# Performance work log

Hardware: AMD Instinct MI355X
Metric: run time of the kernel (lower is better)

The kernel has to match this reference:

```python
import jax, jax.numpy as jnp
import numpy as np

N = 50000; E = 200000; H = 128; L = 3; T = 2; FOUT = 64
G = 1000; NP = 3; ATOM_V = 64; BOND_V = 8
EPS = 1e-5
_DEG_HIST = np.array([0., 50000., 75000., 50000., 25000.])
# PyG PNAConv: avg_deg['log'] = sum(hist[d] * log(d+1)) / num_nodes
AVG_DEG_LOG = float((np.log(np.arange(5) + 1.0) * _DEG_HIST).sum() / _DEG_HIST.sum())


def _bn(v, g, b):
    # training-mode BatchNorm1d (biased variance), eps=1e-5
    mu = v.mean(0)
    var = ((v - mu) ** 2).mean(0)
    return (v - mu) * jax.lax.rsqrt(var + EPS) * g + b


def setup_inputs() -> dict:
    key = jax.random.key(0)
    ks = jax.random.split(key, 16)
    def nrm(k, shape, fan):
        return (jax.random.normal(k, shape, dtype=jnp.float32) / np.sqrt(fan)).astype(jnp.float32)
    return {
        'x': jax.random.randint(ks[0], (N, 9), 0, ATOM_V),
        'edge_index': jax.random.randint(ks[1], (2, E), 0, N),
        'batch': jnp.sort(jax.random.randint(ks[2], (N,), 0, G)),
        'edge_attr_idx': jax.random.randint(ks[3], (E, 3), 0, BOND_V),
        'atom_emb': nrm(ks[4], (9, ATOM_V, H), H),
        'bond_emb': nrm(ks[5], (3, BOND_V, H), H),
        'edge_W': nrm(ks[6], (L, H, H), H), 'edge_b': jnp.zeros((L, H), jnp.float32),
        'pre_W': nrm(ks[7], (L, T, 3 * H, H), 3 * H), 'pre_b': jnp.zeros((L, T, H), jnp.float32),
        'post_W': nrm(ks[8], (L, T, 13 * H, FOUT), 13 * H), 'post_b': jnp.zeros((L, T, FOUT), jnp.float32),
        'lin_W': nrm(ks[9], (L, H, H), H), 'lin_b': jnp.zeros((L, H), jnp.float32),
        'bn_g': jnp.ones((L, H), jnp.float32), 'bn_b': jnp.zeros((L, H), jnp.float32),
        'mlp_W': nrm(ks[10], (2, H, H), H), 'mlp_b': jnp.zeros((2, H), jnp.float32),
        'mlp_g': jnp.ones((2, H), jnp.float32), 'mlp_be': jnp.zeros((2, H), jnp.float32),
        'hW1': nrm(ks[11], (H, H // 2), H), 'hb1': jnp.zeros((H // 2,), jnp.float32),
        'hg1': jnp.ones((H // 2,), jnp.float32), 'hbe1': jnp.zeros((H // 2,), jnp.float32),
        'hW2': nrm(ks[12], (H // 2, H // 4), H // 2), 'hb2': jnp.zeros((H // 4,), jnp.float32),
        'hg2': jnp.ones((H // 4,), jnp.float32), 'hbe2': jnp.zeros((H // 4,), jnp.float32),
        'hW3': nrm(ks[13], (H // 4, NP), H // 4), 'hb3': jnp.zeros((NP,), jnp.float32),
    }


def reference(x, edge_index, batch, edge_attr_idx, atom_emb, bond_emb,
              edge_W, edge_b, pre_W, pre_b, post_W, post_b, lin_W, lin_b,
              bn_g, bn_b, mlp_W, mlp_b, mlp_g, mlp_be,
              hW1, hb1, hg1, hbe1, hW2, hb2, hg2, hbe2, hW3, hb3):
    # encoders: sum of per-feature embeddings (OGB Atom/Bond encoder)
    h = atom_emb[jnp.arange(9), x].sum(1)               # [N,H]
    e = bond_emb[jnp.arange(3), edge_attr_idx].sum(1)   # [E,H]
    src, dst = edge_index[0], edge_index[1]
    cnt = jax.ops.segment_sum(jnp.ones((E,), jnp.float32), dst, N)
    deg = jnp.maximum(cnt, 1.0)[:, None, None]          # clamp(1), as in PyG scalers
    amp = jnp.log(deg + 1.0) / AVG_DEG_LOG
    att = AVG_DEG_LOG / jnp.log(deg + 1.0)
    has = (cnt > 0)[:, None, None]
    for l in range(L):
        ea = e @ edge_W[l] + edge_b[l]                                  # [E,H]
        msg_in = jnp.concatenate([h[dst], h[src], ea], -1)              # [E,3H]
        m = jnp.einsum('ef,tfh->eth', msg_in, pre_W[l]) + pre_b[l]      # [E,T,H]
        s1 = jax.ops.segment_sum(m, dst, N)
        s2 = jax.ops.segment_sum(m * m, dst, N)
        mean = s1 / deg
        std = jnp.sqrt(jax.nn.relu(s2 / deg - mean * mean) + EPS)
        mn = jnp.where(has, jax.ops.segment_min(m, dst, N), 0.0)
        mx = jnp.where(has, jax.ops.segment_max(m, dst, N), 0.0)
        agg = jnp.concatenate([mean, mn, mx, std], -1)                  # [N,T,4H]
        scaled = jnp.concatenate([agg, agg * amp, agg * att], -1)       # [N,T,12H]
        upd = jnp.concatenate(
            [jnp.broadcast_to(h[:, None, :], (N, T, H)), scaled], -1)   # [N,T,13H]
        o = jnp.einsum('ntf,tfo->nto', upd, post_W[l]) + post_b[l]      # [N,T,FOUT]
        o = o.reshape(N, T * FOUT) @ lin_W[l] + lin_b[l]                # [N,H]
        h = jax.nn.relu(_bn(o, bn_g[l], bn_b[l]))
    g = jax.ops.segment_sum(h, batch, G)                                # [G,H]
    for i in range(2):
        g = jax.nn.relu(_bn(g @ mlp_W[i] + mlp_b[i], mlp_g[i], mlp_be[i]))
    g = jax.nn.relu(_bn(g @ hW1 + hb1, hg1, hbe1))
    g = jax.nn.relu(_bn(g @ hW2 + hb2, hg2, hbe2))
    return g @ hW3 + hb3                                                # [G,NP]
```

## Files before the change

### kernel.cpp

```cpp
#include <hip/hip_runtime.h>
#include <math.h>


#define NN 50000
#define NE 200000
#define HD 128
#define NG 1000
#define EPSV 1e-5f
#define ALOGC 1.1330197327247628f

#define AP 1288
#define OP 136
#define ECAP 512
#define SCB 49

typedef __bf16 bf16x8 __attribute__((ext_vector_type(8)));
typedef float f32x4 __attribute__((ext_vector_type(4)));

__device__ __forceinline__ unsigned short f2bf(float f) {
    unsigned int u = __float_as_uint(f);
    unsigned int r = (u + 0x7FFFu + ((u >> 16) & 1u)) >> 16;
    return (unsigned short)r;
}
__device__ __forceinline__ float bf2f(unsigned short h) {
    return __uint_as_float((unsigned int)h << 16);
}

__global__ void k_fill(float* __restrict__ o, float v, int n) {
    int i = blockIdx.x * 256 + threadIdx.x;
    if (i < n) o[i] = v;
}

__global__ void k_zero(float* __restrict__ z, int n) {
    int i = blockIdx.x * 256 + threadIdx.x;
    if (i < n) z[i] = 0.f;
}

__global__ void k_encode_nodes(const int* __restrict__ x, const float* __restrict__ aemb,
                               float* __restrict__ h) {
    int n = blockIdx.x, c = threadIdx.x;
    __shared__ int xi[9];
    if (c < 9) xi[c] = x[n * 9 + c];
    __syncthreads();
    float acc = 0.f;
#pragma unroll
    for (int f = 0; f < 9; ++f) acc += aemb[(f * 64 + xi[f]) * HD + c];
    h[(size_t)n * HD + c] = acc;
}

__global__ void k_count(const int* __restrict__ dst, int* __restrict__ cnt) {
    int e = blockIdx.x * 256 + threadIdx.x;
    if (e < NE) atomicAdd(&cnt[dst[e]], 1);
}

__global__ __launch_bounds__(1024) void k_scanA(const int* __restrict__ cnt,
                                                int* __restrict__ sc, int* __restrict__ tot) {
    __shared__ int buf[1024];
    int tid = threadIdx.x;
    int i = blockIdx.x * 1024 + tid;
    int v = (i < NN) ? cnt[i] : 0;
    buf[tid] = v;
    __syncthreads();
    for (int s = 1; s < 1024; s <<= 1) {
        int t = (tid >= s) ? buf[tid - s] : 0;
        __syncthreads();
        buf[tid] += t;
        __syncthreads();
    }
    if (i < NN) sc[i] = buf[tid];
    if (tid == 1023) tot[blockIdx.x] = buf[1023];
}

__global__ void k_scanB(const int* __restrict__ tot, int* __restrict__ offb) {
    if (threadIdx.x == 0) {
        int run = 0;
        for (int b = 0; b < SCB; ++b) { offb[b] = run; run += tot[b]; }
    }
}

__global__ __launch_bounds__(1024) void k_scanC(
    const int* __restrict__ cnt, const int* __restrict__ sc, const int* __restrict__ offb,
    int* __restrict__ rowptr, float* __restrict__ ampv, float* __restrict__ attv) {
    int i = blockIdx.x * 1024 + threadIdx.x;
    if (i == 0) rowptr[0] = 0;
    if (i < NN) {
        rowptr[i + 1] = offb[blockIdx.x] + sc[i];
        int v = cnt[i];
        float dg = (float)(v > 0 ? v : 1);
        float lg = logf(dg + 1.0f);
        ampv[i] = lg / ALOGC;
        attv[i] = ALOGC / lg;
    }
}

__global__ void k_scatter(const int* __restrict__ dst, const int* __restrict__ rowptr,
                          int* __restrict__ fill, int* __restrict__ eperm) {
    int e = blockIdx.x * 256 + threadIdx.x;
    if (e < NE) {
        int d = dst[e];
        int pos = rowptr[d] + atomicAdd(&fill[d], 1);
        eperm[pos] = e;
    }
}

__global__ void k_eprep(const int* __restrict__ ei, const int* __restrict__ eai,
                        const int* __restrict__ eperm, int* __restrict__ precs) {
    int p = blockIdx.x * 256 + threadIdx.x;
    if (p < NE) {
        int e = eperm[p];
        int cidx = eai[e * 3] | (eai[e * 3 + 1] << 3) | (eai[e * 3 + 2] << 6);
        precs[p] = ei[e] | (cidx << 17);
    }
}

__global__ void k_fold(const float* __restrict__ edge_W, const float* __restrict__ edge_b,
                       const float* __restrict__ pre_W, const float* __restrict__ pre_b,
                       float* __restrict__ cW, float* __restrict__ tb) {
    int l = blockIdx.y;
    int k = blockIdx.x;
    int tj = threadIdx.x;
    int t = tj >> 7, j = tj & 127;
    const float* pw = pre_W + ((size_t)(l * 2 + t) * 384 + 256) * 128 + j;
    if (k < 128) {
        const float* ew = edge_W + ((size_t)l * 128 + k) * 128;
        float acc = 0.f;
        for (int i = 0; i < 128; ++i) acc += ew[i] * pw[i * 128];
        cW[((size_t)l * 128 + k) * 256 + tj] = acc;
    } else {
        const float* eb = edge_b + l * 128;
        float acc = pre_b[(l * 2 + t) * 128 + j];
        for (int i = 0; i < 128; ++i) acc += eb[i] * pw[i * 128];
        tb[l * 256 + tj] = acc;
    }
}

__global__ void k_bond(const float* __restrict__ bemb, const float* __restrict__ cW,
                       float* __restrict__ bondc) {
    int v = blockIdx.x, f = blockIdx.y, l = blockIdx.z;
    int tj = threadIdx.x;
    const float* src = bemb + (size_t)(f * 8 + v) * 128;
    const float* w = cW + (size_t)l * 128 * 256;
    float acc = 0.f;
    for (int i = 0; i < 128; ++i) acc += src[i] * w[i * 256 + tj];
    bondc[(((size_t)l * 3 + f) * 8 + v) * 256 + tj] = acc;
}

__global__ void k_bcomb(const float* __restrict__ bondc, float* __restrict__ bcomb) {
    int ci = blockIdx.x, l = blockIdx.y, tj = threadIdx.x;
    const float* base = bondc + (size_t)l * 3 * 8 * 256;
    float v = base[((0 * 8) + (ci & 7)) * 256 + tj]
            + base[((1 * 8) + ((ci >> 3) & 7)) * 256 + tj]
            + base[((2 * 8) + (ci >> 6)) * 256 + tj];
    bcomb[((size_t)l * 512 + ci) * 256 + tj] = v;
}

__global__ void k_pack(const float* __restrict__ W, int N, int NT,
                       unsigned short* __restrict__ pk) {
    int blk = blockIdx.x;
    int kstep = blk / NT, nt = blk - kstep * NT;
    int lane = threadIdx.x;
    int kb = kstep * 32 + (lane >> 4) * 8;
    int col = nt * 16 + (lane & 15);
    unsigned short tmp[8];
#pragma unroll
    for (int i = 0; i < 8; ++i) tmp[i] = f2bf(W[(size_t)(kb + i) * N + col]);
    *(uint4*)(pk + ((size_t)blk * 64 + lane) * 8) = *(uint4*)tmp;
}

__global__ void k_pack_pre(const float* __restrict__ preW,
                           unsigned short* __restrict__ phi,
                           unsigned short* __restrict__ plo) {
    int b = blockIdx.x;
    int kstep = b >> 5, nt = b & 31;
    int lane = threadIdx.x;
    int q = lane >> 4, nc = lane & 15;
    int col = nt * 16 + nc;
    int t = (col >> 7) & 1;
    int jcol = col & 127;
    int fbase = (col < 256) ? 0 : 128;
    unsigned short hi[8], lo[8];
#pragma unroll
    for (int i = 0; i < 8; ++i) {
        int k = kstep * 32 + q * 8 + i;
        float w = preW[((size_t)t * 384 + fbase + k) * 128 + jcol];
        unsigned short h16 = f2bf(w);
        hi[i] = h16;
        lo[i] = f2bf(w - bf2f(h16));
    }
    size_t base = ((size_t)b * 64 + lane) * 8;
    *(uint4*)(phi + base) = *(uint4*)hi;
    *(uint4*)(plo + base) = *(uint4*)lo;
}

__device__ __forceinline__ void pre_mfma_body(
    const unsigned short* __restrict__ ah, const unsigned short* __restrict__ al,
    const unsigned short* __restrict__ phi, const unsigned short* __restrict__ plo,
    const float* __restrict__ tb, int n0, int tid,
    float* __restrict__ hzd, float* __restrict__ hzs) {
    int lane = tid & 63, w = tid >> 6;
    int q = lane >> 4, nc = lane & 15;
    f32x4 acc[8];
#pragma unroll
    for (int j = 0; j < 8; ++j) acc[j] = (f32x4){0.f, 0.f, 0.f, 0.f};
#pragma unroll
    for (int kk = 0; kk < 4; ++kk) {
        bf16x8 Ahi = *(const bf16x8*)(ah + nc * 136 + kk * 32 + q * 8);
        bf16x8 Alo = *(const bf16x8*)(al + nc * 136 + kk * 32 + q * 8);
#pragma unroll
        for (int j = 0; j < 8; ++j) {
            int nt = w * 8 + j;
            size_t base = ((size_t)(kk * 32 + nt) * 64 + lane) * 8;
            bf16x8 Bhi = *(const bf16x8*)(phi + base);
            bf16x8 Blo = *(const bf16x8*)(plo + base);
            acc[j] = __builtin_amdgcn_mfma_f32_16x16x32_bf16(Ahi, Bhi, acc[j], 0, 0, 0);
            acc[j] = __builtin_amdgcn_mfma_f32_16x16x32_bf16(Ahi, Blo, acc[j], 0, 0, 0);
            acc[j] = __builtin_amdgcn_mfma_f32_16x16x32_bf16(Alo, Bhi, acc[j], 0, 0, 0);
        }
    }
#pragma unroll
    for (int j = 0; j < 8; ++j) {
        int col = (w * 8 + j) * 16 + nc;
#pragma unroll
        for (int reg = 0; reg < 4; ++reg) {
            int row = n0 + q * 4 + reg;
            if (col < 256) hzd[(size_t)row * 256 + col] = acc[j][reg] + tb[col];
            else           hzs[(size_t)row * 256 + (col - 256)] = acc[j][reg];
        }
    }
}

__global__ __launch_bounds__(256) void k_pre_m(
    const float* __restrict__ h,
    const unsigned short* __restrict__ phi, const unsigned short* __restrict__ plo,
    const float* __restrict__ tb,
    float* __restrict__ hzd, float* __restrict__ hzs) {
    __shared__ __align__(16) unsigned short ah[16 * 136];
    __shared__ __align__(16) unsigned short al[16 * 136];
    int n0 = blockIdx.x * 16;
    int tid = threadIdx.x;
    {
        int node = tid >> 4, cg = (tid & 15) * 8;
        const float* hs = h + (size_t)(n0 + node) * HD + cg;
        float4 v0 = *(const float4*)(hs);
        float4 v1 = *(const float4*)(hs + 4);
        float vv[8] = {v0.x, v0.y, v0.z, v0.w, v1.x, v1.y, v1.z, v1.w};
        unsigned short hh[8], ll[8];
#pragma unroll
        for (int i = 0; i < 8; ++i) {
            hh[i] = f2bf(vv[i]);
            ll[i] = f2bf(vv[i] - bf2f(hh[i]));
        }
        *(uint4*)(ah + node * 136 + cg) = *(uint4*)hh;
        *(uint4*)(al + node * 136 + cg) = *(uint4*)ll;
    }
    __syncthreads();
    pre_mfma_body(ah, al, phi, plo, tb, n0, tid, hzd, hzs);
}

__global__ __launch_bounds__(256) void k_bnpre(
    const float* __restrict__ o2, const float* __restrict__ stats,
    const float* __restrict__ g, const float* __restrict__ b,
    const unsigned short* __restrict__ phi, const unsigned short* __restrict__ plo,
    const float* __restrict__ tb,
    float* __restrict__ h, float* __restrict__ hzd, float* __restrict__ hzs) {
    __shared__ __align__(16) unsigned short ah[16 * 136];
    __shared__ __align__(16) unsigned short al[16 * 136];
    int n0 = blockIdx.x * 16;
    int tid = threadIdx.x;
    {
        int node = tid >> 4, cg = (tid & 15) * 8;
        int n = n0 + node;
        const float* os = o2 + (size_t)n * HD + cg;
        float4 v0 = *(const float4*)(os);
        float4 v1 = *(const float4*)(os + 4);
        float vv[8] = {v0.x, v0.y, v0.z, v0.w, v1.x, v1.y, v1.z, v1.w};
        unsigned short hh[8], ll[8];
        float ou[8];
#pragma unroll
        for (int i = 0; i < 8; ++i) {
            int c = cg + i;
            float mu = stats[c] * (1.f / NN);
            float var = stats[128 + c] * (1.f / NN) - mu * mu;
            float val = (vv[i] - mu) * rsqrtf(var + EPSV) * g[c] + b[c];
            val = fmaxf(val, 0.f);
            ou[i] = val;
            hh[i] = f2bf(val);
            ll[i] = f2bf(val - bf2f(hh[i]));
        }
        float* hd = h + (size_t)n * HD + cg;
        *(float4*)(hd) = make_float4(ou[0], ou[1], ou[2], ou[3]);
        *(float4*)(hd + 4) = make_float4(ou[4], ou[5], ou[6], ou[7]);
        *(uint4*)(ah + node * 136 + cg) = *(uint4*)hh;
        *(uint4*)(al + node * 136 + cg) = *(uint4*)ll;
    }
    __syncthreads();
    pre_mfma_body(ah, al, phi, plo, tb, n0, tid, hzd, hzs);
}

__global__ __launch_bounds__(256) void k_post(
    const float* __restrict__ h,
    const float* __restrict__ hzd, const float* __restrict__ hzs,
    const int* __restrict__ rowptr, const int* __restrict__ precs,
    const float* __restrict__ bcomb,
    const float* __restrict__ ampv, const float* __restrict__ attv,
    const unsigned short* __restrict__ pkPost,
    const float* __restrict__ postb,
    const unsigned short* __restrict__ pkLin,
    const float* __restrict__ linb,
    float* __restrict__ o2, float* __restrict__ stats) {
    __shared__ __align__(16) unsigned short a_lds[16 * AP];
    __shared__ __align__(16) unsigned short o_lds[16 * OP];
    __shared__ int es[ECAP];
    __shared__ float s_amp[16], s_att[16];
    int n0 = blockIdx.x * 16;
    int tid = threadIdx.x;

    int pbase = rowptr[n0];
    int ecount = rowptr[n0 + 16] - pbase;
    for (int i = tid; i < ecount && i < ECAP; i += 256) es[i] = precs[pbase + i];
    {
        int node = tid >> 4, cg = (tid & 15) * 8;
        const float* hs = h + (size_t)(n0 + node) * HD + cg;
        float4 v0 = *(const float4*)(hs);
        float4 v1 = *(const float4*)(hs + 4);
        unsigned short* d0 = a_lds + node * AP + cg;
        unsigned short* d1 = d0 + 640;
        unsigned short bb[8];
        bb[0] = f2bf(v0.x); bb[1] = f2bf(v0.y); bb[2] = f2bf(v0.z); bb[3] = f2bf(v0.w);
        bb[4] = f2bf(v1.x); bb[5] = f2bf(v1.y); bb[6] = f2bf(v1.z); bb[7] = f2bf(v1.w);
#pragma unroll
        for (int i = 0; i < 8; ++i) { d0[i] = bb[i]; d1[i] = bb[i]; }
    }
    if (tid < 16) { s_amp[tid] = ampv[n0 + tid]; s_att[tid] = attv[n0 + tid]; }
    __syncthreads();

    {
        int wv = tid >> 6, lane = tid & 63;
        int cc = lane * 4;
        int tt = cc >> 7, jj = cc & 127;
        bool incap = (ecount <= ECAP);
        const float4 Z4 = make_float4(0.f, 0.f, 0.f, 0.f);
        for (int i = 0; i < 4; ++i) {
            int r = wv * 4 + i;
            int n = n0 + r;
            int p0 = rowptr[n], p1 = rowptr[n + 1];
            float4 hd = *(const float4*)(hzd + (size_t)n * 256 + cc);
            float4 s1 = Z4, s2 = Z4;
            float4 mn = make_float4(3.4e38f, 3.4e38f, 3.4e38f, 3.4e38f);
            float4 mx = make_float4(-3.4e38f, -3.4e38f, -3.4e38f, -3.4e38f);
            for (int p = p0; p < p1; ++p) {
                int rec = incap ? es[p - pbase] : precs[p];
                int sp = rec & 131071;
                int ci = rec >> 17;
                float4 vs = *(const float4*)(hzs + (size_t)sp * 256 + cc);
                float4 bc = *(const float4*)(bcomb + (size_t)ci * 256 + cc);
                float wx = vs.x + bc.x, wy = vs.y + bc.y, wz = vs.z + bc.z, ww = vs.w + bc.w;
                s1.x += wx; s1.y += wy; s1.z += wz; s1.w += ww;
                s2.x += wx * wx; s2.y += wy * wy; s2.z += wz * wz; s2.w += ww * ww;
                mn.x = fminf(mn.x, wx); mn.y = fminf(mn.y, wy);
                mn.z = fminf(mn.z, wz); mn.w = fminf(mn.w, ww);
                mx.x = fmaxf(mx.x, wx); mx.y = fmaxf(mx.y, wy);
                mx.z = fmaxf(mx.z, wz); mx.w = fmaxf(mx.w, ww);
            }
            int cnt = p1 - p0;
            float inv = 1.f / (float)(cnt > 0 ? cnt : 1);
            float4 mw, stdv, mean;
            mw.x = s1.x * inv; mw.y = s1.y * inv; mw.z = s1.z * inv; mw.w = s1.w * inv;
            stdv.x = sqrtf(fmaxf(s2.x * inv - mw.x * mw.x, 0.f) + EPSV);
            stdv.y = sqrtf(fmaxf(s2.y * inv - mw.y * mw.y, 0.f) + EPSV);
            stdv.z = sqrtf(fmaxf(s2.z * inv - mw.z * mw.z, 0.f) + EPSV);
            stdv.w = sqrtf(fmaxf(s2.w * inv - mw.w * mw.w, 0.f) + EPSV);
            if (cnt > 0) {
                mean.x = hd.x + mw.x; mean.y = hd.y + mw.y;
                mean.z = hd.z + mw.z; mean.w = hd.w + mw.w;
                mn.x += hd.x; mn.y += hd.y; mn.z += hd.z; mn.w += hd.w;
                mx.x += hd.x; mx.y += hd.y; mx.z += hd.z; mx.w += hd.w;
            } else {
                mean = Z4; mn = Z4; mx = Z4;
            }
            unsigned short* d = a_lds + r * AP + tt * 640 + 128 + jj;
            d[0] = f2bf(mean.x); d[1] = f2bf(mean.y); d[2] = f2bf(mean.z); d[3] = f2bf(mean.w);
            d += 128; d[0] = f2bf(mn.x); d[1] = f2bf(mn.y); d[2] = f2bf(mn.z); d[3] = f2bf(mn.w);
            d += 128; d[0] = f2bf(mx.x); d[1] = f2bf(mx.y); d[2] = f2bf(mx.z); d[3] = f2bf(mx.w);
            d += 128; d[0] = f2bf(stdv.x); d[1] = f2bf(stdv.y); d[2] = f2bf(stdv.z); d[3] = f2bf(stdv.w);
        }
    }
    __syncthreads();

    {
        int lane = tid & 63;
        int w = tid >> 6;
        int t = w >> 1;
        int ntb = (w & 1) * 2;
        int q = lane >> 4, nc = lane & 15;
        const unsigned short* arow = a_lds + (size_t)nc * AP + t * 640 + q * 8;
        const unsigned short* pkt = pkPost + (size_t)t * 106496;
        f32x4 aP0 = {0.f, 0.f, 0.f, 0.f}, aP1 = {0.f, 0.f, 0.f, 0.f};
        f32x4 aA0 = {0.f, 0.f, 0.f, 0.f}, aA1 = {0.f, 0.f, 0.f, 0.f};
        f32x4 aT0 = {0.f, 0.f, 0.f, 0.f}, aT1 = {0.f, 0.f, 0.f, 0.f};
        for (int kk = 0; kk < 20; ++kk) {
            bf16x8 af = *(const bf16x8*)(arow + kk * 32);
            const unsigned short* pb = pkt + ((size_t)(kk * 4 + ntb) * 64 + lane) * 8;
            aP0 = __builtin_amdgcn_mfma_f32_16x16x32_bf16(af, *(const bf16x8*)(pb), aP0, 0, 0, 0);
            aP1 = __builtin_amdgcn_mfma_f32_16x16x32_bf16(af, *(const bf16x8*)(pb + 512), aP1, 0, 0, 0);
            if (kk >= 4) {
                const unsigned short* pa = pkt + ((size_t)((kk + 16) * 4 + ntb) * 64 + lane) * 8;
                aA0 = __builtin_amdgcn_mfma_f32_16x16x32_bf16(af, *(const bf16x8*)(pa), aA0, 0, 0, 0);
                aA1 = __builtin_amdgcn_mfma_f32_16x16x32_bf16(af, *(const bf16x8*)(pa + 512), aA1, 0, 0, 0);
                const unsigned short* pt = pkt + ((size_t)((kk + 32) * 4 + ntb) * 64 + lane) * 8;
                aT0 = __builtin_amdgcn_mfma_f32_16x16x32_bf16(af, *(const bf16x8*)(pt), aT0, 0, 0, 0);
                aT1 = __builtin_amdgcn_mfma_f32_16x16x32_bf16(af, *(const bf16x8*)(pt + 512), aT1, 0, 0, 0);
            }
        }
#pragma unroll
        for (int u = 0; u < 2; ++u) {
            int nt = ntb + u;
            int col = t * 64 + nt * 16 + nc;
            float pbia = postb[t * 64 + nt * 16 + nc];
            f32x4 P = u ? aP1 : aP0;
            f32x4 A = u ? aA1 : aA0;
            f32x4 T = u ? aT1 : aT0;
#pragma unroll
            for (int reg = 0; reg < 4; ++reg) {
                int mrow = q * 4 + reg;
                float val = P[reg] + s_amp[mrow] * A[reg] + s_att[mrow] * T[reg] + pbia;
                o_lds[mrow * OP + col] = f2bf(val);
            }
        }
    }
    __syncthreads();

    {
        int lane = tid & 63;
        int w = tid >> 6;
        int ntb = w * 2;
        int q = lane >> 4, nc = lane & 15;
        const unsigned short* arow = o_lds + (size_t)nc * OP + q * 8;
        f32x4 L0 = {0.f, 0.f, 0.f, 0.f}, L1 = {0.f, 0.f, 0.f, 0.f};
#pragma unroll
        for (int kk = 0; kk < 4; ++kk) {
            bf16x8 af = *(const bf16x8*)(arow + kk * 32);
            const unsigned short* pb = pkLin + ((size_t)(kk * 8 + ntb) * 64 + lane) * 8;
            L0 = __builtin_amdgcn_mfma_f32_16x16x32_bf16(af, *(const bf16x8*)(pb), L0, 0, 0, 0);
            L1 = __builtin_amdgcn_mfma_f32_16x16x32_bf16(af, *(const bf16x8*)(pb + 512), L1, 0, 0, 0);
        }
#pragma unroll
        for (int u = 0; u < 2; ++u) {
            int col = (ntb + u) * 16 + nc;
            float lb = linb[col];
            f32x4 L = u ? L1 : L0;
            float ps = 0.f, pss = 0.f;
#pragma unroll
            for (int reg = 0; reg < 4; ++reg) {
                int mrow = q * 4 + reg;
                float v = L[reg] + lb;
                o2[(size_t)(n0 + mrow) * HD + col] = v;
                ps += v; pss += v * v;
            }
            ps += __shfl_down(ps, 16); ps += __shfl_down(ps, 32);
            pss += __shfl_down(pss, 16); pss += __shfl_down(pss, 32);
            if (q == 0) {
                atomicAdd(&stats[col], ps);
                atomicAdd(&stats[128 + col], pss);
            }
        }
    }
}

__global__ void k_bn_relu(const float* __restrict__ o2, const float* __restrict__ stats,
                          const float* __restrict__ g, const float* __restrict__ b,
                          float* __restrict__ h) {
    int idx = blockIdx.x * 256 + threadIdx.x;
    int c = idx & 127;
    float mu = stats[c] * (1.f / NN);
    float var = stats[128 + c] * (1.f / NN) - mu * mu;
    float v = (o2[idx] - mu) * rsqrtf(var + EPSV) * g[c] + b[c];
    h[idx] = fmaxf(v, 0.f);
}

__global__ void k_pool(const float* __restrict__ h, const int* __restrict__ batch,
                       float* __restrict__ g0) {
    int c = threadIdx.x;
    int nbase = blockIdx.x * 64;
    float run = 0.f; int cur = -1;
    for (int i = 0; i < 64; ++i) {
        int n = nbase + i;
        if (n >= NN) break;
        int bb = batch[n];
        if (bb != cur) {
            if (cur >= 0) atomicAdd(&g0[(size_t)cur * HD + c], run);
            cur = bb; run = 0.f;
        }
        run += h[(size_t)n * HD + c];
    }
    if (cur >= 0) atomicAdd(&g0[(size_t)cur * HD + c], run);
}

__global__ void k_head_gemm(const float* __restrict__ x, const float* __restrict__ W,
                            const float* __restrict__ b, float* __restrict__ y,
                            float* __restrict__ stats, int K, int Kout) {
    int row = blockIdx.x;
    int col = threadIdx.x;
    if (col >= Kout) return;
    float acc = b[col];
    for (int k = 0; k < K; k += 4) {
        float4 xv = *(const float4*)(x + (size_t)row * K + k);
        acc += xv.x * W[(k + 0) * Kout + col] + xv.y * W[(k + 1) * Kout + col]
             + xv.z * W[(k + 2) * Kout + col] + xv.w * W[(k + 3) * Kout + col];
    }
    y[(size_t)row * Kout + col] = acc;
    if (stats) {
        atomicAdd(&stats[col], acc);
        atomicAdd(&stats[Kout + col], acc * acc);
    }
}

__global__ __launch_bounds__(128) void k_head_fused(
    const float* __restrict__ y_in, const float* __restrict__ stats_in,
    const float* __restrict__ g, const float* __restrict__ b,
    const float* __restrict__ W, const float* __restrict__ bias,
    float* __restrict__ y_out, float* __restrict__ stats_out, int Kin, int Kout) {
    __shared__ float row[128];
    int r = blockIdx.x, tid = threadIdx.x;
    if (tid < Kin) {
        float mu = stats_in[tid] * (1.f / NG);
        float var = stats_in[Kin + tid] * (1.f / NG) - mu * mu;
        float v = (y_in[(size_t)r * Kin + tid] - mu) * rsqrtf(var + EPSV) * g[tid] + b[tid];
        row[tid] = fmaxf(v, 0.f);
    }
    __syncthreads();
    if (tid < Kout) {
        float acc = bias[tid];
        for (int k = 0; k < Kin; ++k) acc += row[k] * W[(size_t)k * Kout + tid];
        y_out[(size_t)r * Kout + tid] = acc;
        if (stats_out) {
            atomicAdd(&stats_out[tid], acc);
            atomicAdd(&stats_out[Kout + tid], acc * acc);
        }
    }
}

extern "C" void kernel_launch(void* const* d_in, const int* in_sizes, int n_in,
                              void* d_out, int out_size, void* d_ws, size_t ws_size,
                              hipStream_t stream) {
    const int*   x        = (const int*)  d_in[0];
    const int*   ei       = (const int*)  d_in[1];
    const int*   batch    = (const int*)  d_in[2];
    const int*   eai      = (const int*)  d_in[3];
    const float* atom_emb = (const float*)d_in[4];
    const float* bond_emb = (const float*)d_in[5];
    const float* edge_W   = (const float*)d_in[6];
    const float* edge_b   = (const float*)d_in[7];
    const float* pre_W    = (const float*)d_in[8];
    const float* pre_b    = (const float*)d_in[9];
    const float* post_W   = (const float*)d_in[10];
    const float* post_b   = (const float*)d_in[11];
    const float* lin_W    = (const float*)d_in[12];
    const float* lin_b    = (const float*)d_in[13];
    const float* bn_g     = (const float*)d_in[14];
    const float* bn_b     = (const float*)d_in[15];
    const float* mlp_W    = (const float*)d_in[16];
    const float* mlp_b    = (const float*)d_in[17];
    const float* mlp_g    = (const float*)d_in[18];
    const float* mlp_be   = (const float*)d_in[19];
    const float* hW1 = (const float*)d_in[20]; const float* hb1  = (const float*)d_in[21];
    const float* hg1 = (const float*)d_in[22]; const float* hbe1 = (const float*)d_in[23];
    const float* hW2 = (const float*)d_in[24]; const float* hb2  = (const float*)d_in[25];
    const float* hg2 = (const float*)d_in[26]; const float* hbe2 = (const float*)d_in[27];
    const float* hW3 = (const float*)d_in[28]; const float* hb3  = (const float*)d_in[29];
    float* out = (float*)d_out;
    (void)n_in; (void)in_sizes;

    char* p = (char*)d_ws;
    size_t off = 0;
    auto alloc = [&](size_t bytes) -> char* {
        char* r = p + off;
        off += (bytes + 255) & ~(size_t)255;
        return r;
    };
    float* h     = (float*)alloc((size_t)NN * HD * 4);
    float* o2    = (float*)alloc((size_t)NN * HD * 4);
    float* hzd   = (float*)alloc((size_t)NN * 256 * 4);
    float* hzs   = (float*)alloc((size_t)NN * 256 * 4);
    float* ampv  = (float*)alloc((size_t)NN * 4);
    float* attv  = (float*)alloc((size_t)NN * 4);
    int*   rowptr= (int*)  alloc((size_t)(NN + 1) * 4);
    int*   eperm = (int*)  alloc((size_t)NE * 4);
    int*   precs = (int*)  alloc((size_t)NE * 4);
    int*   sc    = (int*)  alloc((size_t)NN * 4);
    int*   stot  = (int*)  alloc((size_t)SCB * 4);
    int*   soff  = (int*)  alloc((size_t)SCB * 4);
    float* cW    = (float*)alloc((size_t)3 * 128 * 256 * 4);
    float* tbb   = (float*)alloc((size_t)3 * 256 * 4);
    float* bondc = (float*)alloc((size_t)3 * 3 * 8 * 256 * 4);
    float* bcomb = (float*)alloc((size_t)3 * 512 * 256 * 4);
    unsigned short* pkPost  = (unsigned short*)alloc((size_t)3 * 2 * 106496 * 2);
    unsigned short* pkLin   = (unsigned short*)alloc((size_t)3 * 16384 * 2);
    unsigned short* pkPreHi = (unsigned short*)alloc((size_t)3 * 65536 * 2);
    unsigned short* pkPreLo = (unsigned short*)alloc((size_t)3 * 65536 * 2);
    float* gA    = (float*)alloc((size_t)NG * HD * 4);
    float* gB    = (float*)alloc((size_t)NG * HD * 4);
    char* z0 = p + off;
    int*   cnt   = (int*)  alloc((size_t)NN * 4);
    int*   fill  = (int*)  alloc((size_t)NN * 4);
    float* stats = (float*)alloc((size_t)3 * 256 * 4);
    float* hstats= (float*)alloc((size_t)4 * 256 * 4);
    float* g0    = (float*)alloc((size_t)NG * HD * 4);
    size_t zwords = (size_t)((p + off) - z0) / 4;

    if (off > ws_size) {
        k_fill<<<(out_size + 255) / 256, 256, 0, stream>>>(out, (float)ws_size, out_size);
        return;
    }

    k_zero<<<(int)((zwords + 255) / 256), 256, 0, stream>>>((float*)z0, (int)zwords);
    k_encode_nodes<<<NN, 128, 0, stream>>>(x, atom_emb, h);
    k_count<<<(NE + 255) / 256, 256, 0, stream>>>(ei + NE, cnt);
    k_scanA<<<SCB, 1024, 0, stream>>>(cnt, sc, stot);
    k_scanB<<<1, 64, 0, stream>>>(stot, soff);
    k_scanC<<<SCB, 1024, 0, stream>>>(cnt, sc, soff, rowptr, ampv, attv);
    k_scatter<<<(NE + 255) / 256, 256, 0, stream>>>(ei + NE, rowptr, fill, eperm);
    k_eprep<<<(NE + 255) / 256, 256, 0, stream>>>(ei, eai, eperm, precs);
    k_fold<<<dim3(129, 3), 256, 0, stream>>>(edge_W, edge_b, pre_W, pre_b, cW, tbb);
    k_bond<<<dim3(8, 3, 3), 256, 0, stream>>>(bond_emb, cW, bondc);
    k_bcomb<<<dim3(512, 3), 256, 0, stream>>>(bondc, bcomb);
    for (int l = 0; l < 3; ++l) {
        for (int t = 0; t < 2; ++t)
            k_pack<<<52 * 4, 64, 0, stream>>>(post_W + ((size_t)l * 2 + t) * 1664 * 64, 64, 4,
                                              pkPost + ((size_t)l * 2 + t) * 106496);
        k_pack<<<4 * 8, 64, 0, stream>>>(lin_W + (size_t)l * 128 * 128, 128, 8,
                                         pkLin + (size_t)l * 16384);
        k_pack_pre<<<128, 64, 0, stream>>>(pre_W + (size_t)l * 2 * 384 * 128,
                                           pkPreHi + (size_t)l * 65536,
                                           pkPreLo + (size_t)l * 65536);
    }

    for (int l = 0; l < 3; ++l) {
        if (l == 0) {
            k_pre_m<<<NN / 16, 256, 0, stream>>>(h, pkPreHi, pkPreLo, tbb, hzd, hzs);
        } else {
            k_bnpre<<<NN / 16, 256, 0, stream>>>(o2, stats + (l - 1) * 256,
                bn_g + (l - 1) * 128, bn_b + (l - 1) * 128,
                pkPreHi + (size_t)l * 65536, pkPreLo + (size_t)l * 65536,
                tbb + l * 256, h, hzd, hzs);
        }
        k_post<<<NN / 16, 256, 0, stream>>>(h, hzd, hzs, rowptr, precs,
            bcomb + (size_t)l * 512 * 256,
            ampv, attv,
            pkPost + (size_t)l * 2 * 106496, post_b + l * 2 * 64,
            pkLin + (size_t)l * 16384, lin_b + l * 128,
            o2, stats + l * 256);
    }
    k_bn_relu<<<(NN * HD) / 256, 256, 0, stream>>>(o2, stats + 2 * 256,
        bn_g + 2 * 128, bn_b + 2 * 128, h);

    k_pool<<<(NN + 63) / 64, 128, 0, stream>>>(h, batch, g0);

    k_head_gemm<<<NG, 128, 0, stream>>>(g0, mlp_W, mlp_b, gA, hstats, 128, 128);
    k_head_fused<<<NG, 128, 0, stream>>>(gA, hstats, mlp_g, mlp_be,
        mlp_W + 128 * 128, mlp_b + 128, gB, hstats + 256, 128, 128);
    k_head_fused<<<NG, 128, 0, stream>>>(gB, hstats + 256, mlp_g + 128, mlp_be + 128,
        hW1, hb1, gA, hstats + 512, 128, 64);
    k_head_fused<<<NG, 128, 0, stream>>>(gA, hstats + 512, hg1, hbe1,
        hW2, hb2, gB, hstats + 768, 64, 32);
    k_head_fused<<<NG, 128, 0, stream>>>(gB, hstats + 768, hg2, hbe2,
        hW3, hb3, out, (float*)nullptr, 32, 3);
}
```

Measured before the change: 976.7 us.

## Use split-bf16 hi/lo weights in post and lin GEMMs, merge packing kernels

The post and lin weights are now packed as bf16 hi/lo pairs, and k_post issues extra MFMAs per step so the products keep near-fp32 accuracy. The lin input is kept in fp32 in LDS and split into hi/lo on the fly. The separate pack launches are merged into one k_packall kernel, and node encoding is vectorised to float4 with 8 nodes per block. This mainly raises accuracy at the cost of doubling or tripling MFMA work and weight traffic in the hot k_post kernel. The launch merge and encoding vectorisation only trim small overheads.

```diff
diff --git a/kernel.cpp b/kernel.cpp
--- a/kernel.cpp
+++ b/kernel.cpp
@@ -10,7 +10,7 @@
 #define ALOGC 1.1330197327247628f
 
 #define AP 1288
-#define OP 136
+#define OPF 132
 #define ECAP 512
 #define SCB 49
 
@@ -36,16 +36,21 @@
     if (i < n) z[i] = 0.f;
 }
 
-__global__ void k_encode_nodes(const int* __restrict__ x, const float* __restrict__ aemb,
-                               float* __restrict__ h) {
-    int n = blockIdx.x, c = threadIdx.x;
-    __shared__ int xi[9];
-    if (c < 9) xi[c] = x[n * 9 + c];
+__global__ __launch_bounds__(256) void k_encode_nodes(
+    const int* __restrict__ x, const float* __restrict__ aemb, float* __restrict__ h) {
+    __shared__ int xi[8][9];
+    int nb = blockIdx.x * 8;
+    int tid = threadIdx.x;
+    if (tid < 72) xi[tid / 9][tid % 9] = x[nb * 9 + tid];
     __syncthreads();
-    float acc = 0.f;
-#pragma unroll
-    for (int f = 0; f < 9; ++f) acc += aemb[(f * 64 + xi[f]) * HD + c];
-    h[(size_t)n * HD + c] = acc;
+    int node = tid >> 5, c4 = (tid & 31) * 4;
+    float4 acc = make_float4(0.f, 0.f, 0.f, 0.f);
+#pragma unroll
+    for (int f = 0; f < 9; ++f) {
+        float4 e = *(const float4*)(aemb + (size_t)(f * 64 + xi[node][f]) * HD + c4);
+        acc.x += e.x; acc.y += e.y; acc.z += e.z; acc.w += e.w;
+    }
+    *(float4*)(h + (size_t)(nb + node) * HD + c4) = acc;
 }
 
 __global__ void k_count(const int* __restrict__ dst, int* __restrict__ cnt) {
@@ -154,42 +159,70 @@
     bcomb[((size_t)l * 512 + ci) * 256 + tj] = v;
 }
 
-__global__ void k_pack(const float* __restrict__ W, int N, int NT,
-                       unsigned short* __restrict__ pk) {
-    int blk = blockIdx.x;
+__device__ __forceinline__ void pack_body2(const float* __restrict__ W, int N, int NT,
+                                           unsigned short* __restrict__ pkh,
+                                           unsigned short* __restrict__ pkl,
+                                           int blk, int lane) {
     int kstep = blk / NT, nt = blk - kstep * NT;
-    int lane = threadIdx.x;
     int kb = kstep * 32 + (lane >> 4) * 8;
     int col = nt * 16 + (lane & 15);
-    unsigned short tmp[8];
-#pragma unroll
-    for (int i = 0; i < 8; ++i) tmp[i] = f2bf(W[(size_t)(kb + i) * N + col]);
-    *(uint4*)(pk + ((size_t)blk * 64 + lane) * 8) = *(uint4*)tmp;
-}
-
-__global__ void k_pack_pre(const float* __restrict__ preW,
-                           unsigned short* __restrict__ phi,
-                           unsigned short* __restrict__ plo) {
+    unsigned short th[8], tl[8];
+#pragma unroll
+    for (int i = 0; i < 8; ++i) {
+        float w = W[(size_t)(kb + i) * N + col];
+        unsigned short hh = f2bf(w);
+        th[i] = hh;
+        tl[i] = f2bf(w - bf2f(hh));
+    }
+    size_t base = ((size_t)blk * 64 + lane) * 8;
+    *(uint4*)(pkh + base) = *(uint4*)th;
+    *(uint4*)(pkl + base) = *(uint4*)tl;
+}
+
+__global__ __launch_bounds__(64) void k_packall(
+    const float* __restrict__ post_W, const float* __restrict__ lin_W,
+    const float* __restrict__ pre_W,
+    unsigned short* __restrict__ pkPostHi, unsigned short* __restrict__ pkPostLo,
+    unsigned short* __restrict__ pkLinHi, unsigned short* __restrict__ pkLinLo,
+    unsigned short* __restrict__ pkPreHi, unsigned short* __restrict__ pkPreLo) {
     int b = blockIdx.x;
-    int kstep = b >> 5, nt = b & 31;
     int lane = threadIdx.x;
-    int q = lane >> 4, nc = lane & 15;
-    int col = nt * 16 + nc;
-    int t = (col >> 7) & 1;
-    int jcol = col & 127;
-    int fbase = (col < 256) ? 0 : 128;
-    unsigned short hi[8], lo[8];
-#pragma unroll
-    for (int i = 0; i < 8; ++i) {
-        int k = kstep * 32 + q * 8 + i;
-        float w = preW[((size_t)t * 384 + fbase + k) * 128 + jcol];
-        unsigned short h16 = f2bf(w);
-        hi[i] = h16;
-        lo[i] = f2bf(w - bf2f(h16));
-    }
-    size_t base = ((size_t)b * 64 + lane) * 8;
-    *(uint4*)(phi + base) = *(uint4*)hi;
-    *(uint4*)(plo + base) = *(uint4*)lo;
+    if (b < 1248) {
+        int l = b / 416, rem = b % 416;
+        int t = rem / 208, blk = rem % 208;
+        size_t off = ((size_t)l * 2 + t) * 106496;
+        pack_body2(post_W + ((size_t)l * 2 + t) * 1664 * 64, 64, 4,
+                   pkPostHi + off, pkPostLo + off, blk, lane);
+    } else if (b < 1344) {
+        int idx = b - 1248;
+        int l = idx / 32, blk = idx % 32;
+        pack_body2(lin_W + (size_t)l * 128 * 128, 128, 8,
+                   pkLinHi + (size_t)l * 16384, pkLinLo + (size_t)l * 16384, blk, lane);
+    } else {
+        int idx = b - 1344;
+        int l = idx / 128, bb = idx % 128;
+        const float* preW = pre_W + (size_t)l * 2 * 384 * 128;
+        unsigned short* phi = pkPreHi + (size_t)l * 65536;
+        unsigned short* plo = pkPreLo + (size_t)l * 65536;
+        int kstep = bb >> 5, nt = bb & 31;
+        int q = lane >> 4, nc = lane & 15;
+        int col = nt * 16 + nc;
+        int t = (col >> 7) & 1;
+        int jcol = col & 127;
+        int fbase = (col < 256) ? 0 : 128;
+        unsigned short hi[8], lo[8];
+#pragma unroll
+        for (int i = 0; i < 8; ++i) {
+            int k = kstep * 32 + q * 8 + i;
+            float w = preW[((size_t)t * 384 + fbase + k) * 128 + jcol];
+            unsigned short h16 = f2bf(w);
+            hi[i] = h16;
+            lo[i] = f2bf(w - bf2f(h16));
+        }
+        size_t base = ((size_t)bb * 64 + lane) * 8;
+        *(uint4*)(phi + base) = *(uint4*)hi;
+        *(uint4*)(plo + base) = *(uint4*)lo;
+    }
 }
 
 __device__ __forceinline__ void pre_mfma_body(
@@ -303,13 +336,13 @@
     const int* __restrict__ rowptr, const int* __restrict__ precs,
     const float* __restrict__ bcomb,
     const float* __restrict__ ampv, const float* __restrict__ attv,
-    const unsigned short* __restrict__ pkPost,
+    const unsigned short* __restrict__ pkPostHi, const unsigned short* __restrict__ pkPostLo,
     const float* __restrict__ postb,
-    const unsigned short* __restrict__ pkLin,
+    const unsigned short* __restrict__ pkLinHi, const unsigned short* __restrict__ pkLinLo,
     const float* __restrict__ linb,
     float* __restrict__ o2, float* __restrict__ stats) {
     __shared__ __align__(16) unsigned short a_lds[16 * AP];
-    __shared__ __align__(16) unsigned short o_lds[16 * OP];
+    __shared__ __align__(16) float o_f[16 * OPF];
     __shared__ int es[ECAP];
     __shared__ float s_amp[16], s_att[16];
     int n0 = blockIdx.x * 16;
@@ -394,22 +427,30 @@
         int ntb = (w & 1) * 2;
         int q = lane >> 4, nc = lane & 15;
         const unsigned short* arow = a_lds + (size_t)nc * AP + t * 640 + q * 8;
-        const unsigned short* pkt = pkPost + (size_t)t * 106496;
+        size_t toff = (size_t)t * 106496;
+        const unsigned short* pkh = pkPostHi + toff;
+        const unsigned short* pkl = pkPostLo + toff;
         f32x4 aP0 = {0.f, 0.f, 0.f, 0.f}, aP1 = {0.f, 0.f, 0.f, 0.f};
         f32x4 aA0 = {0.f, 0.f, 0.f, 0.f}, aA1 = {0.f, 0.f, 0.f, 0.f};
         f32x4 aT0 = {0.f, 0.f, 0.f, 0.f}, aT1 = {0.f, 0.f, 0.f, 0.f};
         for (int kk = 0; kk < 20; ++kk) {
             bf16x8 af = *(const bf16x8*)(arow + kk * 32);
-            const unsigned short* pb = pkt + ((size_t)(kk * 4 + ntb) * 64 + lane) * 8;
-            aP0 = __builtin_amdgcn_mfma_f32_16x16x32_bf16(af, *(const bf16x8*)(pb), aP0, 0, 0, 0);
-            aP1 = __builtin_amdgcn_mfma_f32_16x16x32_bf16(af, *(const bf16x8*)(pb + 512), aP1, 0, 0, 0);
+            size_t ib = ((size_t)(kk * 4 + ntb) * 64 + lane) * 8;
+            aP0 = __builtin_amdgcn_mfma_f32_16x16x32_bf16(af, *(const bf16x8*)(pkh + ib), aP0, 0, 0, 0);
+            aP0 = __builtin_amdgcn_mfma_f32_16x16x32_bf16(af, *(const bf16x8*)(pkl + ib), aP0, 0, 0, 0);
+            aP1 = __builtin_amdgcn_mfma_f32_16x16x32_bf16(af, *(const bf16x8*)(pkh + ib + 512), aP1, 0, 0, 0);
+            aP1 = __builtin_amdgcn_mfma_f32_16x16x32_bf16(af, *(const bf16x8*)(pkl + ib + 512), aP1, 0, 0, 0);
             if (kk >= 4) {
-                const unsigned short* pa = pkt + ((size_t)((kk + 16) * 4 + ntb) * 64 + lane) * 8;
-                aA0 = __builtin_amdgcn_mfma_f32_16x16x32_bf16(af, *(const bf16x8*)(pa), aA0, 0, 0, 0);
-                aA1 = __builtin_amdgcn_mfma_f32_16x16x32_bf16(af, *(const bf16x8*)(pa + 512), aA1, 0, 0, 0);
-                const unsigned short* pt = pkt + ((size_t)((kk + 32) * 4 + ntb) * 64 + lane) * 8;
-                aT0 = __builtin_amdgcn_mfma_f32_16x16x32_bf16(af, *(const bf16x8*)(pt), aT0, 0, 0, 0);
-                aT1 = __builtin_amdgcn_mfma_f32_16x16x32_bf16(af, *(const bf16x8*)(pt + 512), aT1, 0, 0, 0);
+                size_t ia = ((size_t)((kk + 16) * 4 + ntb) * 64 + lane) * 8;
+                aA0 = __builtin_amdgcn_mfma_f32_16x16x32_bf16(af, *(const bf16x8*)(pkh + ia), aA0, 0, 0, 0);
+                aA0 = __builtin_amdgcn_mfma_f32_16x16x32_bf16(af, *(const bf16x8*)(pkl + ia), aA0, 0, 0, 0);
+                aA1 = __builtin_amdgcn_mfma_f32_16x16x32_bf16(af, *(const bf16x8*)(pkh + ia + 512), aA1, 0, 0, 0);
+                aA1 = __builtin_amdgcn_mfma_f32_16x16x32_bf16(af, *(const bf16x8*)(pkl + ia + 512), aA1, 0, 0, 0);
+                size_t it = ((size_t)((kk + 32) * 4 + ntb) * 64 + lane) * 8;
+                aT0 = __builtin_amdgcn_mfma_f32_16x16x32_bf16(af, *(const bf16x8*)(pkh + it), aT0, 0, 0, 0);
+                aT0 = __builtin_amdgcn_mfma_f32_16x16x32_bf16(af, *(const bf16x8*)(pkl + it), aT0, 0, 0, 0);
+                aT1 = __builtin_amdgcn_mfma_f32_16x16x32_bf16(af, *(const bf16x8*)(pkh + it + 512), aT1, 0, 0, 0);
+                aT1 = __builtin_amdgcn_mfma_f32_16x16x32_bf16(af, *(const bf16x8*)(pkl + it + 512), aT1, 0, 0, 0);
             }
         }
 #pragma unroll
@@ -423,8 +464,7 @@
 #pragma unroll
             for (int reg = 0; reg < 4; ++reg) {
                 int mrow = q * 4 + reg;
-                float val = P[reg] + s_amp[mrow] * A[reg] + s_att[mrow] * T[reg] + pbia;
-                o_lds[mrow * OP + col] = f2bf(val);
+                o_f[mrow * OPF + col] = P[reg] + s_amp[mrow] * A[reg] + s_att[mrow] * T[reg] + pbia;
             }
         }
     }
@@ -435,14 +475,32 @@
         int w = tid >> 6;
         int ntb = w * 2;
         int q = lane >> 4, nc = lane & 15;
-        const unsigned short* arow = o_lds + (size_t)nc * OP + q * 8;
+        const float* arow = o_f + (size_t)nc * OPF + q * 8;
         f32x4 L0 = {0.f, 0.f, 0.f, 0.f}, L1 = {0.f, 0.f, 0.f, 0.f};
 #pragma unroll
         for (int kk = 0; kk < 4; ++kk) {
-            bf16x8 af = *(const bf16x8*)(arow + kk * 32);
-            const unsigned short* pb = pkLin + ((size_t)(kk * 8 + ntb) * 64 + lane) * 8;
-            L0 = __builtin_amdgcn_mfma_f32_16x16x32_bf16(af, *(const bf16x8*)(pb), L0, 0, 0, 0);
-            L1 = __builtin_amdgcn_mfma_f32_16x16x32_bf16(af, *(const bf16x8*)(pb + 512), L1, 0, 0, 0);
+            float4 a0 = *(const float4*)(arow + kk * 32);
+            float4 a1 = *(const float4*)(arow + kk * 32 + 4);
+            float vv[8] = {a0.x, a0.y, a0.z, a0.w, a1.x, a1.y, a1.z, a1.w};
+            unsigned short hh[8], ll[8];
+#pragma unroll
+            for (int i = 0; i < 8; ++i) {
+                hh[i] = f2bf(vv[i]);
+                ll[i] = f2bf(vv[i] - bf2f(hh[i]));
+            }
+            bf16x8 Ahi = *(const bf16x8*)hh;
+            bf16x8 Alo = *(const bf16x8*)ll;
+            size_t ib = ((size_t)(kk * 8 + ntb) * 64 + lane) * 8;
+            bf16x8 B0h = *(const bf16x8*)(pkLinHi + ib);
+            bf16x8 B0l = *(const bf16x8*)(pkLinLo + ib);
+            bf16x8 B1h = *(const bf16x8*)(pkLinHi + ib + 512);
+            bf16x8 B1l = *(const bf16x8*)(pkLinLo + ib + 512);
+            L0 = __builtin_amdgcn_mfma_f32_16x16x32_bf16(Ahi, B0h, L0, 0, 0, 0);
+            L0 = __builtin_amdgcn_mfma_f32_16x16x32_bf16(Alo, B0h, L0, 0, 0, 0);
+            L0 = __builtin_amdgcn_mfma_f32_16x16x32_bf16(Ahi, B0l, L0, 0, 0, 0);
+            L1 = __builtin_amdgcn_mfma_f32_16x16x32_bf16(Ahi, B1h, L1, 0, 0, 0);
+            L1 = __builtin_amdgcn_mfma_f32_16x16x32_bf16(Alo, B1h, L1, 0, 0, 0);
+            L1 = __builtin_amdgcn_mfma_f32_16x16x32_bf16(Ahi, B1l, L1, 0, 0, 0);
         }
 #pragma unroll
         for (int u = 0; u < 2; ++u) {
@@ -594,10 +652,12 @@
     float* tbb   = (float*)alloc((size_t)3 * 256 * 4);
     float* bondc = (float*)alloc((size_t)3 * 3 * 8 * 256 * 4);
     float* bcomb = (float*)alloc((size_t)3 * 512 * 256 * 4);
-    unsigned short* pkPost  = (unsigned short*)alloc((size_t)3 * 2 * 106496 * 2);
-    unsigned short* pkLin   = (unsigned short*)alloc((size_t)3 * 16384 * 2);
-    unsigned short* pkPreHi = (unsigned short*)alloc((size_t)3 * 65536 * 2);
-    unsigned short* pkPreLo = (unsigned short*)alloc((size_t)3 * 65536 * 2);
+    unsigned short* pkPostHi = (unsigned short*)alloc((size_t)3 * 2 * 106496 * 2);
+    unsigned short* pkPostLo = (unsigned short*)alloc((size_t)3 * 2 * 106496 * 2);
+    unsigned short* pkLinHi  = (unsigned short*)alloc((size_t)3 * 16384 * 2);
+    unsigned short* pkLinLo  = (unsigned short*)alloc((size_t)3 * 16384 * 2);
+    unsigned short* pkPreHi  = (unsigned short*)alloc((size_t)3 * 65536 * 2);
+    unsigned short* pkPreLo  = (unsigned short*)alloc((size_t)3 * 65536 * 2);
     float* gA    = (float*)alloc((size_t)NG * HD * 4);
     float* gB    = (float*)alloc((size_t)NG * HD * 4);
     char* z0 = p + off;
@@ -614,7 +674,7 @@
     }
 
     k_zero<<<(int)((zwords + 255) / 256), 256, 0, stream>>>((float*)z0, (int)zwords);
-    k_encode_nodes<<<NN, 128, 0, stream>>>(x, atom_emb, h);
+    k_encode_nodes<<<NN / 8, 256, 0, stream>>>(x, atom_emb, h);
     k_count<<<(NE + 255) / 256, 256, 0, stream>>>(ei + NE, cnt);
     k_scanA<<<SCB, 1024, 0, stream>>>(cnt, sc, stot);
     k_scanB<<<1, 64, 0, stream>>>(stot, soff);
@@ -624,16 +684,8 @@
     k_fold<<<dim3(129, 3), 256, 0, stream>>>(edge_W, edge_b, pre_W, pre_b, cW, tbb);
     k_bond<<<dim3(8, 3, 3), 256, 0, stream>>>(bond_emb, cW, bondc);
     k_bcomb<<<dim3(512, 3), 256, 0, stream>>>(bondc, bcomb);
-    for (int l = 0; l < 3; ++l) {
-        for (int t = 0; t < 2; ++t)
-            k_pack<<<52 * 4, 64, 0, stream>>>(post_W + ((size_t)l * 2 + t) * 1664 * 64, 64, 4,
-                                              pkPost + ((size_t)l * 2 + t) * 106496);
-        k_pack<<<4 * 8, 64, 0, stream>>>(lin_W + (size_t)l * 128 * 128, 128, 8,
-                                         pkLin + (size_t)l * 16384);
-        k_pack_pre<<<128, 64, 0, stream>>>(pre_W + (size_t)l * 2 * 384 * 128,
-                                           pkPreHi + (size_t)l * 65536,
-                                           pkPreLo + (size_t)l * 65536);
-    }
+    k_packall<<<1728, 64, 0, stream>>>(post_W, lin_W, pre_W,
+        pkPostHi, pkPostLo, pkLinHi, pkLinLo, pkPreHi, pkPreLo);
 
     for (int l = 0; l < 3; ++l) {
         if (l == 0) {
@@ -647,8 +699,10 @@
         k_post<<<NN / 16, 256, 0, stream>>>(h, hzd, hzs, rowptr, precs,
             bcomb + (size_t)l * 512 * 256,
             ampv, attv,
-            pkPost + (size_t)l * 2 * 106496, post_b + l * 2 * 64,
-            pkLin + (size_t)l * 16384, lin_b + l * 128,
+            pkPostHi + (size_t)l * 2 * 106496, pkPostLo + (size_t)l * 2 * 106496,
+            post_b + l * 2 * 64,
+            pkLinHi + (size_t)l * 16384, pkLinLo + (size_t)l * 16384,
+            lin_b + l * 128,
             o2, stats + l * 256);
     }
     k_bn_relu<<<(NN * HD) / 256, 256, 0, stream>>>(o2, stats + 2 * 256,
```

Result: no change. 981.4 us (+0.5%).
